# Kernel tuning notes

Hardware: AMD Instinct MI355X
Metric: run time of the kernel (lower is better)

Reference implementation:

```python
import jax, jax.numpy as jnp
import numpy as np

B, N, N_HEAD, HDIM = 16, 512, 8, 64


def setup_inputs() -> dict:
    key = jax.random.key(0)
    kq, kk, kv, kg = jax.random.split(key, 4)
    q = jax.random.normal(kq, (B, N, N_HEAD, HDIM), dtype=jnp.float32)
    k = jax.random.normal(kk, (B, N, N_HEAD, HDIM), dtype=jnp.float32)
    v = jax.random.normal(kv, (B, N, N_HEAD, HDIM), dtype=jnp.float32)
    geo_f = jax.random.normal(kg, (B, N, N), dtype=jnp.float32)
    return {"q": q, "k": k, "v": v, "geo_f": geo_f}


def reference(q, k, v, geo_f):
    # q,k,v: [B,N,H,D]; geo_f: [B,N,N]
    D = q.shape[-1]
    scale = D ** (-0.5)  # total_weight = qk_weight / scale  (i.e. * sqrt(D))
    # pairwise_distance = negative squared Euclidean distance between per-head
    # query/key vectors: -||q_i - k_j||^2 = 2 q.k - ||q||^2 - ||k||^2
    qk = jnp.einsum('bnhd,bmhd->bhnm', q, k)            # [B,H,N,N]
    q2 = jnp.sum(q * q, axis=-1).transpose(0, 2, 1)     # [B,H,N]
    k2 = jnp.sum(k * k, axis=-1).transpose(0, 2, 1)     # [B,H,N]
    dist = 2.0 * qk - q2[..., :, None] - k2[..., None, :]
    total = (dist + geo_f[:, None, :, :]) / scale       # geo bias broadcast over heads
    # global max subtraction in the source is a no-op under softmax; softmax is stable anyway
    w = jax.nn.softmax(total, axis=-1)                  # [B,H,N,N]
    # weighted sum over keys m (dropout p=0.0 -> identity)
    out = jnp.einsum('bmhd,bhnm->bnhd', v, w)           # [B,N,H,D]
    return out
```

## Files before the change

kernel.cpp:

```cpp
#include <hip/hip_runtime.h>
#include <hip/hip_bf16.h>

#define BB 16
#define NN 512
#define NH 8
#define DD 64
#define QBLK 64
#define WAVES 4
#define KBLK 128
#define NCHUNK 4
#define NT 32
#define TPC 8

typedef __attribute__((ext_vector_type(8))) short bf16x8;
typedef __attribute__((ext_vector_type(4))) float f32x4;

__device__ __forceinline__ unsigned short f2bf(float f) {
    unsigned int u = __float_as_uint(f);
    u += 0x7fffu + ((u >> 16) & 1u);
    return (unsigned short)(u >> 16);
}
__device__ __forceinline__ float bf2f(unsigned short h) {
    return __uint_as_float(((unsigned int)h) << 16);
}

__global__ __launch_bounds__(256, 2) void geo_attn_kernel(
    const float* __restrict__ Q, const float* __restrict__ K,
    const float* __restrict__ V, const float* __restrict__ GEO,
    float* __restrict__ OUT)
{
    const int qt  = blockIdx.x;
    const int h   = blockIdx.y;
    const int b   = blockIdx.z;
    const int tid = threadIdx.x;
    const int w    = tid >> 6;
    const int lane = tid & 63;
    const int g = lane >> 4;
    const int c = lane & 15;

    __shared__ unsigned short smemA[16384];
    __shared__ float k2p[2][NN];
    __shared__ float rowinv[WAVES][16];

    unsigned short* Khi = smemA;
    unsigned short* Klo = smemA + KBLK*DD;
    unsigned short* vT  = smemA;
    unsigned short* Pld = smemA + DD*KBLK + w*16*KBLK;

    const int qb = qt*QBLK + w*16;

    bf16x8 qhi[2], qlo[2];
    float q2v = 0.f;
    {
        const float* qrow = Q + ((size_t)((b*NN + qb + c)*NH + h))*DD;
        #pragma unroll
        for (int dc = 0; dc < 2; ++dc) {
            float buf[8];
            *(float4*)&buf[0] = *(const float4*)(qrow + dc*32 + g*8);
            *(float4*)&buf[4] = *(const float4*)(qrow + dc*32 + g*8 + 4);
            #pragma unroll
            for (int i = 0; i < 8; ++i) {
                float f = buf[i];
                q2v += f*f;
                unsigned short hu = f2bf(f);
                qhi[dc][i] = (short)hu;
                qlo[dc][i] = (short)f2bf(f - bf2f(hu));
            }
        }
    }
    q2v += __shfl_xor(q2v, 16);
    q2v += __shfl_xor(q2v, 32);

    f32x4 zero4; zero4[0]=0.f; zero4[1]=0.f; zero4[2]=0.f; zero4[3]=0.f;
    f32x4 acc[NT];
    #pragma unroll
    for (int t = 0; t < NT; ++t) acc[t] = zero4;

    #pragma unroll
    for (int c2 = 0; c2 < NCHUNK; ++c2) {
        __syncthreads();
        {
            const int keyl = tid & (KBLK-1);
            const int half = tid >> 7;
            const int d0 = half*32;
            const float* krow = K + ((size_t)((b*NN + c2*KBLK + keyl)*NH + h))*DD + d0;
            float k2s = 0.f;
            #pragma unroll
            for (int jj = 0; jj < 8; ++jj) {
                float4 f4 = *(const float4*)(krow + jj*4);
                float fb[4] = {f4.x, f4.y, f4.z, f4.w};
                unsigned short hu[4], lu[4];
                #pragma unroll
                for (int e = 0; e < 4; ++e) {
                    float f = fb[e];
                    k2s += f*f;
                    hu[e] = f2bf(f);
                    lu[e] = f2bf(f - bf2f(hu[e]));
                }
                int idx = (keyl*DD + d0 + jj*4) ^ ((keyl & 7) << 3);
                *(uint2*)&Khi[idx] = make_uint2((unsigned)hu[0] | ((unsigned)hu[1] << 16),
                                                (unsigned)hu[2] | ((unsigned)hu[3] << 16));
                *(uint2*)&Klo[idx] = make_uint2((unsigned)lu[0] | ((unsigned)lu[1] << 16),
                                                (unsigned)lu[2] | ((unsigned)lu[3] << 16));
            }
            k2p[half][c2*KBLK + keyl] = k2s;
        }
        __syncthreads();
        #pragma unroll
        for (int tl = 0; tl < TPC; ++tl) {
            const int key = tl*16 + c;
            #pragma unroll
            for (int dc = 0; dc < 2; ++dc) {
                int idx = (key*DD + dc*32 + g*8) ^ ((key & 7) << 3);
                bf16x8 kh = *(const bf16x8*)&Khi[idx];
                bf16x8 kl = *(const bf16x8*)&Klo[idx];
                acc[c2*TPC+tl] = __builtin_amdgcn_mfma_f32_16x16x32_bf16(qhi[dc], kh, acc[c2*TPC+tl], 0,0,0);
                acc[c2*TPC+tl] = __builtin_amdgcn_mfma_f32_16x16x32_bf16(qlo[dc], kh, acc[c2*TPC+tl], 0,0,0);
                acc[c2*TPC+tl] = __builtin_amdgcn_mfma_f32_16x16x32_bf16(qhi[dc], kl, acc[c2*TPC+tl], 0,0,0);
            }
        }
    }

    float nq2[4];
    #pragma unroll
    for (int r = 0; r < 4; ++r) nq2[r] = -8.f * __shfl(q2v, g*4 + r);

    const float* geoB = GEO + (size_t)b*NN*NN + (size_t)(qb + 4*g)*NN;

    float mx[4] = {-3e38f, -3e38f, -3e38f, -3e38f};
    #pragma unroll
    for (int t = 0; t < NT; ++t) {
        float kk8 = -8.f * (k2p[0][t*16 + c] + k2p[1][t*16 + c]);
        #pragma unroll
        for (int r = 0; r < 4; ++r) {
            float gv = geoB[(size_t)r*NN + t*16 + c];
            float s = fmaf(16.f, acc[t][r], fmaf(8.f, gv, nq2[r] + kk8));
            acc[t][r] = s;
            mx[r] = fmaxf(mx[r], s);
        }
    }
    #pragma unroll
    for (int r = 0; r < 4; ++r) {
        float mv = mx[r];
        mv = fmaxf(mv, __shfl_xor(mv, 1));
        mv = fmaxf(mv, __shfl_xor(mv, 2));
        mv = fmaxf(mv, __shfl_xor(mv, 4));
        mv = fmaxf(mv, __shfl_xor(mv, 8));
        mx[r] = mv;
    }
    float sm[4] = {0.f, 0.f, 0.f, 0.f};
    #pragma unroll
    for (int t = 0; t < NT; ++t) {
        #pragma unroll
        for (int r = 0; r < 4; ++r) {
            float p = __expf(acc[t][r] - mx[r]);
            acc[t][r] = p;
            sm[r] += p;
        }
    }
    #pragma unroll
    for (int r = 0; r < 4; ++r) {
        float sv = sm[r];
        sv += __shfl_xor(sv, 1);
        sv += __shfl_xor(sv, 2);
        sv += __shfl_xor(sv, 4);
        sv += __shfl_xor(sv, 8);
        sm[r] = sv;
    }
    if (c == 0) {
        #pragma unroll
        for (int r = 0; r < 4; ++r) rowinv[w][4*g + r] = 1.f / sm[r];
    }

    f32x4 oacc[4];
    #pragma unroll
    for (int cb = 0; cb < 4; ++cb) oacc[cb] = zero4;

    #pragma unroll
    for (int c2 = 0; c2 < NCHUNK; ++c2) {
        __syncthreads();
        {
            const int keyl = tid & (KBLK-1);
            const int half = tid >> 7;
            const int d0 = half*32;
            const float* vrow = V + ((size_t)((b*NN + c2*KBLK + keyl)*NH + h))*DD + d0;
            #pragma unroll
            for (int jj = 0; jj < 8; ++jj) {
                float4 f4 = *(const float4*)(vrow + jj*4);
                float fb[4] = {f4.x, f4.y, f4.z, f4.w};
                #pragma unroll
                for (int e = 0; e < 4; ++e) {
                    int d = d0 + jj*4 + e;
                    vT[(d*KBLK + keyl) ^ ((d & 7) << 3)] = f2bf(fb[e]);
                }
            }
        }
        #pragma unroll
        for (int tl = 0; tl < TPC; ++tl) {
            #pragma unroll
            for (int r = 0; r < 4; ++r) {
                int qloc = 4*g + r;
                Pld[(qloc*KBLK + tl*16 + c) ^ ((qloc & 7) << 3)] = f2bf(acc[c2*TPC+tl][r]);
            }
        }
        __syncthreads();
        #pragma unroll
        for (int kc = 0; kc < 4; ++kc) {
            int kb2 = kc*32 + g*8;
            bf16x8 pf = *(const bf16x8*)&Pld[(c*KBLK + kb2) ^ ((c & 7) << 3)];
            #pragma unroll
            for (int cb = 0; cb < 4; ++cb) {
                int d = cb*16 + c;
                bf16x8 vf = *(const bf16x8*)&vT[(d*KBLK + kb2) ^ ((d & 7) << 3)];
                oacc[cb] = __builtin_amdgcn_mfma_f32_16x16x32_bf16(vf, pf, oacc[cb], 0,0,0);
            }
        }
    }

    const float inv = rowinv[w][c];
    float* orow = OUT + ((size_t)((b*NN + qb + c)*NH + h))*DD + 4*g;
    #pragma unroll
    for (int cb = 0; cb < 4; ++cb) {
        float4 ov;
        ov.x = oacc[cb][0] * inv;
        ov.y = oacc[cb][1] * inv;
        ov.z = oacc[cb][2] * inv;
        ov.w = oacc[cb][3] * inv;
        *(float4*)(orow + cb*16) = ov;
    }
}

extern "C" void kernel_launch(void* const* d_in, const int* in_sizes, int n_in,
                              void* d_out, int out_size, void* d_ws, size_t ws_size,
                              hipStream_t stream) {
    const float* q   = (const float*)d_in[0];
    const float* k   = (const float*)d_in[1];
    const float* v   = (const float*)d_in[2];
    const float* geo = (const float*)d_in[3];
    float* out = (float*)d_out;
    dim3 grid(NN/QBLK, NH, BB);
    geo_attn_kernel<<<grid, 256, 0, stream>>>(q, k, v, geo, out);
}
```

Baseline: 158.9 us.

## Split K/V bf16 preprocessing into prep kernel and stream chunks via LDS DMA

Adds a prep kernel that converts K and V once per (batch, head) into pre-swizzled bf16 hi/lo K, transposed V and key norms in workspace. The main kernel then streams 64-key chunks with global_load_lds directly into LDS, including a swizzled geo tile, and uses online softmax instead of holding all 512 scores in registers. The intent is to remove the conversion work repeated by the 8 query-tile blocks and to cut register pressure so occupancy can rise. In exchange it adds a second launch, extra workspace traffic and more barriers per chunk. The old kernel is kept as a fallback when the workspace is too small.

```diff
diff --git a/kernel.cpp b/kernel.cpp
--- a/kernel.cpp
+++ b/kernel.cpp
@@ -7,6 +7,9 @@
 #define DD 64
 #define QBLK 64
 #define WAVES 4
+#define CK 64
+#define NCH 8
+#define TL 4
 #define KBLK 128
 #define NCHUNK 4
 #define NT 32
@@ -23,8 +26,266 @@
 __device__ __forceinline__ float bf2f(unsigned short h) {
     return __uint_as_float(((unsigned int)h) << 16);
 }
-
-__global__ __launch_bounds__(256, 2) void geo_attn_kernel(
+__device__ __forceinline__ void gload16(const void* gsrc, void* lds) {
+    __builtin_amdgcn_global_load_lds(
+        (const __attribute__((address_space(1))) unsigned int*)gsrc,
+        (__attribute__((address_space(3))) unsigned int*)lds, 16, 0, 0);
+}
+
+__global__ __launch_bounds__(256) void geo_prep(
+    const float* __restrict__ K, const float* __restrict__ V,
+    unsigned short* __restrict__ KhiG, unsigned short* __restrict__ KloG,
+    unsigned short* __restrict__ VtG, float* __restrict__ k2G)
+{
+    const int c2 = blockIdx.x;
+    const int h  = blockIdx.y;
+    const int b  = blockIdx.z;
+    const int bh = b*NH + h;
+    const int tid = threadIdx.x;
+    const int lane16 = tid & 15;
+    const int grp    = tid >> 4;
+
+    __shared__ unsigned short Vl[DD*66];
+
+    const size_t kbase = (size_t)bh*(NN*DD) + (size_t)c2*(CK*DD);
+    #pragma unroll
+    for (int kk = 0; kk < 4; ++kk) {
+        const int kl = kk*16 + grp;
+        const float* krow = K + ((size_t)(((b*NN + c2*CK + kl)*NH) + h))*DD + lane16*4;
+        const float* vrow = V + ((size_t)(((b*NN + c2*CK + kl)*NH) + h))*DD + lane16*4;
+        float4 kf = *(const float4*)krow;
+        float4 vf = *(const float4*)vrow;
+        float fb[4] = {kf.x, kf.y, kf.z, kf.w};
+        float vb[4] = {vf.x, vf.y, vf.z, vf.w};
+        unsigned short hu[4], lu[4];
+        float k2s = 0.f;
+        #pragma unroll
+        for (int e = 0; e < 4; ++e) {
+            float f = fb[e];
+            k2s += f*f;
+            hu[e] = f2bf(f);
+            lu[e] = f2bf(f - bf2f(hu[e]));
+            Vl[(lane16*4 + e)*66 + kl] = f2bf(vb[e]);
+        }
+        k2s += __shfl_xor(k2s, 1);
+        k2s += __shfl_xor(k2s, 2);
+        k2s += __shfl_xor(k2s, 4);
+        k2s += __shfl_xor(k2s, 8);
+        if (lane16 == 0) k2G[bh*NN + c2*CK + kl] = k2s;
+        const int pos = (kl*DD + lane16*4) ^ ((kl & 7) << 3);
+        *(uint2*)&KhiG[kbase + pos] = make_uint2((unsigned)hu[0] | ((unsigned)hu[1] << 16),
+                                                 (unsigned)hu[2] | ((unsigned)hu[3] << 16));
+        *(uint2*)&KloG[kbase + pos] = make_uint2((unsigned)lu[0] | ((unsigned)lu[1] << 16),
+                                                 (unsigned)lu[2] | ((unsigned)lu[3] << 16));
+    }
+    __syncthreads();
+    const size_t vbase = ((size_t)bh*NCH + c2)*(DD*CK);
+    #pragma unroll
+    for (int i = 0; i < 4; ++i) {
+        const int gi = tid + 256*i;
+        const int d   = gi >> 4;
+        const int kl4 = (gi & 15) * 4;
+        unsigned short e0 = Vl[d*66 + kl4+0];
+        unsigned short e1 = Vl[d*66 + kl4+1];
+        unsigned short e2 = Vl[d*66 + kl4+2];
+        unsigned short e3 = Vl[d*66 + kl4+3];
+        const int pos = (d*CK + kl4) ^ ((d & 7) << 3);
+        *(uint2*)&VtG[vbase + pos] = make_uint2((unsigned)e0 | ((unsigned)e1 << 16),
+                                                (unsigned)e2 | ((unsigned)e3 << 16));
+    }
+}
+
+__global__ __launch_bounds__(256, 3) void geo_attn_main(
+    const float* __restrict__ Q, const float* __restrict__ GEO,
+    const unsigned short* __restrict__ KhiG, const unsigned short* __restrict__ KloG,
+    const unsigned short* __restrict__ VtG, const float* __restrict__ k2G,
+    float* __restrict__ OUT)
+{
+    const int qt  = blockIdx.x;
+    const int h   = blockIdx.y;
+    const int b   = blockIdx.z;
+    const int bh  = b*NH + h;
+    const int tid = threadIdx.x;
+    const int w    = tid >> 6;
+    const int lane = tid & 63;
+    const int g = lane >> 4;
+    const int c = lane & 15;
+
+    __shared__ unsigned short Khi[CK*DD];
+    __shared__ unsigned short Klo[CK*DD];
+    __shared__ unsigned short vT [DD*CK];
+    __shared__ float geoS[QBLK*CK];
+    __shared__ unsigned short Pld[WAVES*16*CK];
+    __shared__ float k2s[NN];
+    __shared__ float sRow[WAVES][16];
+    __shared__ float rowinv[WAVES][16];
+
+    if (tid < 128) *(float4*)&k2s[tid*4] = *(const float4*)&k2G[(size_t)bh*NN + tid*4];
+
+    const int qb = qt*QBLK + w*16;
+
+    bf16x8 qhi[2], qlo[2];
+    float q2v = 0.f;
+    {
+        const float* qrow = Q + ((size_t)((b*NN + qb + c)*NH + h))*DD;
+        #pragma unroll
+        for (int dc = 0; dc < 2; ++dc) {
+            float buf[8];
+            *(float4*)&buf[0] = *(const float4*)(qrow + dc*32 + g*8);
+            *(float4*)&buf[4] = *(const float4*)(qrow + dc*32 + g*8 + 4);
+            #pragma unroll
+            for (int i = 0; i < 8; ++i) {
+                float f = buf[i];
+                q2v += f*f;
+                unsigned short hu = f2bf(f);
+                qhi[dc][i] = (short)hu;
+                qlo[dc][i] = (short)f2bf(f - bf2f(hu));
+            }
+        }
+    }
+    q2v += __shfl_xor(q2v, 16);
+    q2v += __shfl_xor(q2v, 32);
+    float nq2[4];
+    #pragma unroll
+    for (int r = 0; r < 4; ++r) nq2[r] = -8.f * __shfl(q2v, g*4 + r);
+
+    f32x4 oacc[4];
+    #pragma unroll
+    for (int cb = 0; cb < 4; ++cb) { oacc[cb][0]=0.f; oacc[cb][1]=0.f; oacc[cb][2]=0.f; oacc[cb][3]=0.f; }
+    float m_r[4] = {-3e38f, -3e38f, -3e38f, -3e38f};
+    float l_r[4] = {0.f, 0.f, 0.f, 0.f};
+
+    const char* gKhiB = (const char*)KhiG + (size_t)bh*(NN*DD*2);
+    const char* gKloB = (const char*)KloG + (size_t)bh*(NN*DD*2);
+    const char* gVtB  = (const char*)VtG  + (size_t)bh*(NN*DD*2);
+    const float* geoQ = GEO + (size_t)b*NN*NN + (size_t)(qt*QBLK)*NN;
+
+    for (int ch = 0; ch < NCH; ++ch) {
+        __syncthreads();
+        {
+            const char* srcKhi = gKhiB + ch*(CK*DD*2);
+            const char* srcKlo = gKloB + ch*(CK*DD*2);
+            const char* srcVt  = gVtB  + ch*(CK*DD*2);
+            #pragma unroll
+            for (int i = 0; i < 2; ++i) {
+                const int off = (w*2 + i)*1024;
+                gload16(srcKhi + off + (lane<<4), (char*)Khi + off);
+                gload16(srcKlo + off + (lane<<4), (char*)Klo + off);
+                gload16(srcVt  + off + (lane<<4), (char*)vT  + off);
+            }
+            #pragma unroll
+            for (int i = 0; i < 4; ++i) {
+                const int seg = w*4 + i;
+                const int row = seg*4 + (lane >> 4);
+                const int cg  = (lane & 15) ^ (row & 7);
+                gload16((const void*)(geoQ + (size_t)row*NN + ch*CK + cg*4),
+                        (char*)geoS + seg*1024);
+            }
+        }
+        __syncthreads();
+
+        f32x4 sacc[TL];
+        #pragma unroll
+        for (int tl = 0; tl < TL; ++tl) { sacc[tl][0]=0.f; sacc[tl][1]=0.f; sacc[tl][2]=0.f; sacc[tl][3]=0.f; }
+        #pragma unroll
+        for (int tl = 0; tl < TL; ++tl) {
+            const int key = tl*16 + c;
+            #pragma unroll
+            for (int dc = 0; dc < 2; ++dc) {
+                const int idx = (key*DD + dc*32 + g*8) ^ ((key & 7) << 3);
+                bf16x8 kh = *(const bf16x8*)&Khi[idx];
+                bf16x8 kl = *(const bf16x8*)&Klo[idx];
+                sacc[tl] = __builtin_amdgcn_mfma_f32_16x16x32_bf16(qhi[dc], kh, sacc[tl], 0,0,0);
+                sacc[tl] = __builtin_amdgcn_mfma_f32_16x16x32_bf16(qlo[dc], kh, sacc[tl], 0,0,0);
+                sacc[tl] = __builtin_amdgcn_mfma_f32_16x16x32_bf16(qhi[dc], kl, sacc[tl], 0,0,0);
+            }
+        }
+
+        const int row_base = w*16 + 4*g;
+        float cmax[4] = {-3e38f, -3e38f, -3e38f, -3e38f};
+        #pragma unroll
+        for (int tl = 0; tl < TL; ++tl) {
+            const float kk8 = -8.f * k2s[ch*CK + tl*16 + c];
+            #pragma unroll
+            for (int r = 0; r < 4; ++r) {
+                const int rl = row_base + r;
+                const float gv = geoS[(rl*16 + ((tl*4 + (c>>2)) ^ (rl & 7)))*4 + (c & 3)];
+                float s = fmaf(16.f, sacc[tl][r], fmaf(8.f, gv, nq2[r] + kk8));
+                sacc[tl][r] = s;
+                cmax[r] = fmaxf(cmax[r], s);
+            }
+        }
+        float fac[4];
+        #pragma unroll
+        for (int r = 0; r < 4; ++r) {
+            float mv = cmax[r];
+            mv = fmaxf(mv, __shfl_xor(mv, 1));
+            mv = fmaxf(mv, __shfl_xor(mv, 2));
+            mv = fmaxf(mv, __shfl_xor(mv, 4));
+            mv = fmaxf(mv, __shfl_xor(mv, 8));
+            const float mnew = fmaxf(m_r[r], mv);
+            fac[r] = __expf(m_r[r] - mnew);
+            m_r[r] = mnew;
+        }
+        if (c == 0) {
+            #pragma unroll
+            for (int r = 0; r < 4; ++r) sRow[w][4*g + r] = fac[r];
+        }
+        #pragma unroll
+        for (int r = 0; r < 4; ++r) l_r[r] *= fac[r];
+        #pragma unroll
+        for (int tl = 0; tl < TL; ++tl) {
+            #pragma unroll
+            for (int r = 0; r < 4; ++r) {
+                float p = __expf(sacc[tl][r] - m_r[r]);
+                l_r[r] += p;
+                const int qloc = 4*g + r;
+                Pld[(((w*16 + qloc)*CK) + tl*16 + c) ^ ((qloc & 7) << 3)] = f2bf(p);
+            }
+        }
+        __syncthreads();
+
+        const float sc = sRow[w][c];
+        #pragma unroll
+        for (int cb = 0; cb < 4; ++cb) {
+            oacc[cb][0] *= sc; oacc[cb][1] *= sc; oacc[cb][2] *= sc; oacc[cb][3] *= sc;
+        }
+        #pragma unroll
+        for (int kc = 0; kc < 2; ++kc) {
+            bf16x8 pf = *(const bf16x8*)&Pld[(((w*16 + c)*CK) + kc*32 + g*8) ^ ((c & 7) << 3)];
+            #pragma unroll
+            for (int cb = 0; cb < 4; ++cb) {
+                const int d = cb*16 + c;
+                bf16x8 vfr = *(const bf16x8*)&vT[(d*CK + kc*32 + g*8) ^ ((d & 7) << 3)];
+                oacc[cb] = __builtin_amdgcn_mfma_f32_16x16x32_bf16(vfr, pf, oacc[cb], 0,0,0);
+            }
+        }
+    }
+
+    #pragma unroll
+    for (int r = 0; r < 4; ++r) {
+        float sv = l_r[r];
+        sv += __shfl_xor(sv, 1);
+        sv += __shfl_xor(sv, 2);
+        sv += __shfl_xor(sv, 4);
+        sv += __shfl_xor(sv, 8);
+        if (c == 0) rowinv[w][4*g + r] = 1.f / sv;
+    }
+    __syncthreads();
+    const float inv = rowinv[w][c];
+    float* orow = OUT + ((size_t)((b*NN + qb + c)*NH + h))*DD + 4*g;
+    #pragma unroll
+    for (int cb = 0; cb < 4; ++cb) {
+        float4 ov;
+        ov.x = oacc[cb][0] * inv;
+        ov.y = oacc[cb][1] * inv;
+        ov.z = oacc[cb][2] * inv;
+        ov.w = oacc[cb][3] * inv;
+        *(float4*)(orow + cb*16) = ov;
+    }
+}
+
+__global__ __launch_bounds__(256, 2) void geo_attn_fallback(
     const float* __restrict__ Q, const float* __restrict__ K,
     const float* __restrict__ V, const float* __restrict__ GEO,
     float* __restrict__ OUT)
@@ -40,12 +301,12 @@
 
     __shared__ unsigned short smemA[16384];
     __shared__ float k2p[2][NN];
-    __shared__ float rowinv[WAVES][16];
-
-    unsigned short* Khi = smemA;
-    unsigned short* Klo = smemA + KBLK*DD;
-    unsigned short* vT  = smemA;
-    unsigned short* Pld = smemA + DD*KBLK + w*16*KBLK;
+    __shared__ float rowinvF[WAVES][16];
+
+    unsigned short* KhiF = smemA;
+    unsigned short* KloF = smemA + KBLK*DD;
+    unsigned short* vTF  = smemA;
+    unsigned short* PldF = smemA + DD*KBLK + w*16*KBLK;
 
     const int qb = qt*QBLK + w*16;
 
@@ -84,7 +345,7 @@
             const int half = tid >> 7;
             const int d0 = half*32;
             const float* krow = K + ((size_t)((b*NN + c2*KBLK + keyl)*NH + h))*DD + d0;
-            float k2s = 0.f;
+            float k2sv = 0.f;
             #pragma unroll
             for (int jj = 0; jj < 8; ++jj) {
                 float4 f4 = *(const float4*)(krow + jj*4);
@@ -93,17 +354,17 @@
                 #pragma unroll
                 for (int e = 0; e < 4; ++e) {
                     float f = fb[e];
-                    k2s += f*f;
+                    k2sv += f*f;
                     hu[e] = f2bf(f);
                     lu[e] = f2bf(f - bf2f(hu[e]));
                 }
                 int idx = (keyl*DD + d0 + jj*4) ^ ((keyl & 7) << 3);
-                *(uint2*)&Khi[idx] = make_uint2((unsigned)hu[0] | ((unsigned)hu[1] << 16),
-                                                (unsigned)hu[2] | ((unsigned)hu[3] << 16));
-                *(uint2*)&Klo[idx] = make_uint2((unsigned)lu[0] | ((unsigned)lu[1] << 16),
-                                                (unsigned)lu[2] | ((unsigned)lu[3] << 16));
-            }
-            k2p[half][c2*KBLK + keyl] = k2s;
+                *(uint2*)&KhiF[idx] = make_uint2((unsigned)hu[0] | ((unsigned)hu[1] << 16),
+                                                 (unsigned)hu[2] | ((unsigned)hu[3] << 16));
+                *(uint2*)&KloF[idx] = make_uint2((unsigned)lu[0] | ((unsigned)lu[1] << 16),
+                                                 (unsigned)lu[2] | ((unsigned)lu[3] << 16));
+            }
+            k2p[half][c2*KBLK + keyl] = k2sv;
         }
         __syncthreads();
         #pragma unroll
@@ -112,8 +373,8 @@
             #pragma unroll
             for (int dc = 0; dc < 2; ++dc) {
                 int idx = (key*DD + dc*32 + g*8) ^ ((key & 7) << 3);
-                bf16x8 kh = *(const bf16x8*)&Khi[idx];
-                bf16x8 kl = *(const bf16x8*)&Klo[idx];
+                bf16x8 kh = *(const bf16x8*)&KhiF[idx];
+                bf16x8 kl = *(const bf16x8*)&KloF[idx];
                 acc[c2*TPC+tl] = __builtin_amdgcn_mfma_f32_16x16x32_bf16(qhi[dc], kh, acc[c2*TPC+tl], 0,0,0);
                 acc[c2*TPC+tl] = __builtin_amdgcn_mfma_f32_16x16x32_bf16(qlo[dc], kh, acc[c2*TPC+tl], 0,0,0);
                 acc[c2*TPC+tl] = __builtin_amdgcn_mfma_f32_16x16x32_bf16(qhi[dc], kl, acc[c2*TPC+tl], 0,0,0);
@@ -169,7 +430,7 @@
     }
     if (c == 0) {
         #pragma unroll
-        for (int r = 0; r < 4; ++r) rowinv[w][4*g + r] = 1.f / sm[r];
+        for (int r = 0; r < 4; ++r) rowinvF[w][4*g + r] = 1.f / sm[r];
     }
 
     f32x4 oacc[4];
@@ -191,7 +452,7 @@
                 #pragma unroll
                 for (int e = 0; e < 4; ++e) {
                     int d = d0 + jj*4 + e;
-                    vT[(d*KBLK + keyl) ^ ((d & 7) << 3)] = f2bf(fb[e]);
+                    vTF[(d*KBLK + keyl) ^ ((d & 7) << 3)] = f2bf(fb[e]);
                 }
             }
         }
@@ -200,24 +461,24 @@
             #pragma unroll
             for (int r = 0; r < 4; ++r) {
                 int qloc = 4*g + r;
-                Pld[(qloc*KBLK + tl*16 + c) ^ ((qloc & 7) << 3)] = f2bf(acc[c2*TPC+tl][r]);
+                PldF[(qloc*KBLK + tl*16 + c) ^ ((qloc & 7) << 3)] = f2bf(acc[c2*TPC+tl][r]);
             }
         }
         __syncthreads();
         #pragma unroll
         for (int kc = 0; kc < 4; ++kc) {
             int kb2 = kc*32 + g*8;
-            bf16x8 pf = *(const bf16x8*)&Pld[(c*KBLK + kb2) ^ ((c & 7) << 3)];
+            bf16x8 pf = *(const bf16x8*)&PldF[(c*KBLK + kb2) ^ ((c & 7) << 3)];
             #pragma unroll
             for (int cb = 0; cb < 4; ++cb) {
                 int d = cb*16 + c;
-                bf16x8 vf = *(const bf16x8*)&vT[(d*KBLK + kb2) ^ ((d & 7) << 3)];
+                bf16x8 vf = *(const bf16x8*)&vTF[(d*KBLK + kb2) ^ ((d & 7) << 3)];
                 oacc[cb] = __builtin_amdgcn_mfma_f32_16x16x32_bf16(vf, pf, oacc[cb], 0,0,0);
             }
         }
     }
 
-    const float inv = rowinv[w][c];
+    const float inv = rowinvF[w][c];
     float* orow = OUT + ((size_t)((b*NN + qb + c)*NH + h))*DD + 4*g;
     #pragma unroll
     for (int cb = 0; cb < 4; ++cb) {
@@ -238,6 +499,21 @@
     const float* v   = (const float*)d_in[2];
     const float* geo = (const float*)d_in[3];
     float* out = (float*)d_out;
-    dim3 grid(NN/QBLK, NH, BB);
-    geo_attn_kernel<<<grid, 256, 0, stream>>>(q, k, v, geo, out);
-}
+
+    const size_t IMG = (size_t)BB*NH*NN*DD*2;
+    const size_t need = 3*IMG + (size_t)BB*NH*NN*4;
+
+    if (ws_size >= need) {
+        unsigned short* KhiG = (unsigned short*)d_ws;
+        unsigned short* KloG = (unsigned short*)((char*)d_ws + IMG);
+        unsigned short* VtG  = (unsigned short*)((char*)d_ws + 2*IMG);
+        float*          k2G  = (float*)((char*)d_ws + 3*IMG);
+        dim3 pgrid(NCH, NH, BB);
+        geo_prep<<<pgrid, 256, 0, stream>>>(k, v, KhiG, KloG, VtG, k2G);
+        dim3 grid(NN/QBLK, NH, BB);
+        geo_attn_main<<<grid, 256, 0, stream>>>(q, geo, KhiG, KloG, VtG, k2G, out);
+    } else {
+        dim3 grid(NN/QBLK, NH, BB);
+        geo_attn_fallback<<<grid, 256, 0, stream>>>(q, k, v, geo, out);
+    }
+}
```

New measurement: 154.4 us. 2.8% less time.
